# Performance work log

Hardware: AMD Instinct MI355X
Metric: run time of the kernel (lower is better)

## Reference

```python
import jax, jax.numpy as jnp
import numpy as np

B, N, C, K = 16, 2000, 4, 8
EPS = 1e-5


def setup_inputs() -> dict:
    key = jax.random.key(0)
    ks = jax.random.split(key, 10)
    def p(k, shape, s=0.1):
        return jax.random.normal(k, shape, jnp.float32) * s
    return {
        "data": jax.random.normal(ks[0], (B, 1, N, C), jnp.float32),
        "x": jax.random.normal(ks[1], (B, 1, N, 4), jnp.float32),
        "w1a": p(ks[2], (128, C)), "b1a": jnp.zeros((128,), jnp.float32),
        "w1b": p(ks[3], (128, 128)), "b1b": jnp.zeros((128,), jnp.float32),
        "w2": p(ks[4], (128, 2 * C + 2)), "b2": jnp.zeros((128,), jnp.float32),
        "res_wa": p(ks[5], (4, 128, 128)), "res_ba": jnp.zeros((4, 128), jnp.float32),
        "res_wb": p(ks[6], (4, 128, 128)), "res_bb": jnp.zeros((4, 128), jnp.float32),
        "wl": p(ks[7], (1, 128)), "bl": jnp.zeros((1,), jnp.float32),
    }


def conv1x1(t, w, b):
    # t: [B, Cin, H, W], w: [Cout, Cin]
    return jnp.einsum('bchw,oc->bohw', t, w) + b[None, :, None, None]


def bn(t):
    # training-mode BatchNorm2d, gamma=1 beta=0 (default init)
    m = jnp.mean(t, axis=(0, 2, 3), keepdims=True)
    v = jnp.var(t, axis=(0, 2, 3), keepdims=True)
    return (t - m) * jax.lax.rsqrt(v + EPS)


def instn(t):
    # InstanceNorm2d, affine=False
    m = jnp.mean(t, axis=(2, 3), keepdims=True)
    v = jnp.var(t, axis=(2, 3), keepdims=True)
    return (t - m) * jax.lax.rsqrt(v + EPS)


def res_block(t, wa, ba, wb, bb):
    h = jax.nn.relu(bn(instn(conv1x1(t, wa, ba))))
    h = bn(instn(conv1x1(h, wb, bb)))
    return jax.nn.relu(h + t)


def knn_idx(f, k):
    # f: [B, D, N]; negative squared distance, top-(k+1), drop self
    xx = jnp.sum(f * f, axis=1)                        # [B, N]
    inner = jnp.einsum('bdn,bdm->bnm', f, f)           # [B, N, N]
    pd = 2.0 * inner - xx[:, :, None] - xx[:, None, :]
    idx = jax.lax.top_k(pd, k + 1)[1]                  # [B, N, k+1]
    return idx[:, :, 1:]


def graph_feature(f, idx):
    # f: [B, D, N], idx: [B, N, k] -> [B, 2D, N, k]
    xf = jnp.transpose(f, (0, 2, 1))                   # [B, N, D]
    nb = jax.vmap(lambda a, i: a[i])(xf, idx)          # [B, N, k, D]
    xt = xf[:, :, None, :]
    gf = jnp.concatenate([jnp.broadcast_to(xt, nb.shape), xt - nb], axis=-1)
    return jnp.transpose(gf, (0, 3, 1, 2))


def reference(data, x, w1a, b1a, w1b, b1b, w2, b2,
              res_wa, res_ba, res_wb, res_bb, wl, bl):
    n = data.shape[2]
    t = jnp.transpose(data, (0, 3, 2, 1))              # [B, C, N, 1]

    # self_attention
    h = conv1x1(t, w1a, b1a)
    h = jax.nn.relu(bn(h))
    h = conv1x1(h, w1b, b1b)[..., 0]                   # [B, 128, N]
    h = h / (jnp.linalg.norm(h, axis=1, keepdims=True) + 1e-5)
    A_rowsum = jnp.einsum('bcn,bcm->bm', h, h)         # sum_i A[i, j]
    D = (A_rowsum - 1.0) / n                           # [B, N] (eye subtraction)
    feat = jnp.concatenate(
        [t, jax.nn.relu(jnp.tanh(D))[:, None, :, None]], axis=1)  # [B, C+1, N, 1]

    f = feat[..., 0]                                   # [B, C+1, N]
    idx = knn_idx(f, K)
    g = graph_feature(f, idx)                          # [B, 2C+2, N, K]

    out = jax.nn.relu(bn(conv1x1(g, w2, b2)))          # [B, 128, N, K]
    out = jnp.max(out, axis=-1, keepdims=True)         # [B, 128, N, 1]

    for i in range(4):
        out = res_block(out, res_wa[i], res_ba[i], res_wb[i], res_bb[i])

    logit = conv1x1(out, wl, bl)[:, 0, :, 0]           # [B, N]

    # weighted 8-point
    weights = jax.nn.relu(jnp.tanh(logit))             # [B, N]
    xp = jnp.transpose(x[:, 0], (0, 2, 1))             # [B, 4, N]
    ones = jnp.ones_like(xp[:, 0])
    X = jnp.stack([xp[:, 2] * xp[:, 0], xp[:, 2] * xp[:, 1], xp[:, 2],
                   xp[:, 3] * xp[:, 0], xp[:, 3] * xp[:, 1], xp[:, 3],
                   xp[:, 0], xp[:, 1], ones], axis=1)  # [B, 9, N]
    X = jnp.transpose(X, (0, 2, 1))                    # [B, N, 9]
    XwX = jnp.einsum('bnp,bnq->bpq', X, weights[:, :, None] * X)  # [B, 9, 9]
    _, v = jnp.linalg.eigh(XwX)                        # ascending eigvals
    e_hat = v[:, :, 0]                                 # smallest-eig eigenvector
    e_hat = e_hat / jnp.linalg.norm(e_hat, axis=1, keepdims=True)

    return (D, logit, e_hat)
```

## Files before the change

### kernel.cpp

```cpp
#include <hip/hip_runtime.h>
#include <math.h>

#define BB 16
#define NN 2000
#define CH 128
#define KNN 8
#define JCH 8
#define JSZ 250

__device__ inline float wred(float v) {
    for (int off = 32; off > 0; off >>= 1) v += __shfl_down(v, off, 64);
    return v;
}

__global__ void k_build_t(const float* __restrict__ data, float* __restrict__ t) {
    int i = blockIdx.x * 256 + threadIdx.x;
    if (i >= BB * 4 * NN) return;
    int n = i % NN;
    int c = (i / NN) & 3;
    int b = i / (4 * NN);
    t[i] = data[(b * NN + n) * 4 + c];
}

__global__ void k_conv1(const float* __restrict__ t, const float* __restrict__ w1a,
                        const float* __restrict__ b1a, float* __restrict__ c1) {
    int i = blockIdx.x * 256 + threadIdx.x;
    if (i >= BB * CH * NN) return;
    int n = i % NN;
    int rest = i / NN;
    int o = rest & 127;
    int b = rest >> 7;
    float acc = b1a[o];
    for (int c = 0; c < 4; ++c) acc += w1a[o * 4 + c] * t[(b * 4 + c) * NN + n];
    c1[i] = acc;
}

__global__ void k_chanstats(const float* __restrict__ src, float* __restrict__ chAB) {
    int o = blockIdx.x;
    int tid = threadIdx.x;
    float s = 0.f, ss = 0.f;
    for (int b = 0; b < BB; ++b) {
        const float* p = src + (b * CH + o) * NN;
        for (int n = tid; n < NN; n += 256) { float v = p[n]; s += v; ss += v * v; }
    }
    s = wred(s); ss = wred(ss);
    __shared__ float sh[8];
    int wid = tid >> 6, lane = tid & 63;
    if (lane == 0) { sh[wid] = s; sh[4 + wid] = ss; }
    __syncthreads();
    if (tid == 0) {
        float S0 = sh[0] + sh[1] + sh[2] + sh[3];
        float SS = sh[4] + sh[5] + sh[6] + sh[7];
        float m = S0 / (float)(BB * NN);
        float var = SS / (float)(BB * NN) - m * m;
        float a = rsqrtf(var + 1e-5f);
        chAB[o] = a;
        chAB[CH + o] = -m * a;
    }
}

__global__ __launch_bounds__(256) void k_gemm(const float* __restrict__ X, const float* __restrict__ W,
                                              const float* __restrict__ bias, float* __restrict__ Y,
                                              const float* __restrict__ ab, int mode) {
    int ot = blockIdx.x, by = blockIdx.y;
    int b = by >> 5, nt = by & 31;
    int n0 = nt * 64, o0 = ot * 64;
    int tid = threadIdx.x;
    int tx = tid & 15, ty = tid >> 4;
    __shared__ float Xs[32][64];
    __shared__ float Ws[32][68];
    float acc[4][4] = {};
    for (int jc = 0; jc < 4; ++jc) {
        for (int q = 0; q < 8; ++q) {
            int e = q * 256 + tid;
            int jj = e >> 6, nn = e & 63;
            int j = jc * 32 + jj, n = n0 + nn;
            float v = 0.f;
            if (n < NN) {
                v = X[(b * CH + j) * NN + n];
                if (mode == 1) v = fmaxf(ab[j] * v + ab[CH + j], 0.f);
                else if (mode == 2) { int bc = b * CH + j; v = fmaxf(ab[bc * 2] * v + ab[bc * 2 + 1], 0.f); }
            }
            Xs[jj][nn] = v;
        }
        for (int q = 0; q < 8; ++q) {
            int e = q * 256 + tid;
            int jj = e & 31, oo = e >> 5;
            Ws[jj][oo] = W[(o0 + oo) * CH + jc * 32 + jj];
        }
        __syncthreads();
        for (int jj = 0; jj < 32; ++jj) {
            float4 wv = *(const float4*)&Ws[jj][ty * 4];
            float4 xv = *(const float4*)&Xs[jj][tx * 4];
            float wva[4] = {wv.x, wv.y, wv.z, wv.w};
            float xva[4] = {xv.x, xv.y, xv.z, xv.w};
#pragma unroll
            for (int a = 0; a < 4; ++a)
#pragma unroll
                for (int bq = 0; bq < 4; ++bq) acc[a][bq] += wva[a] * xva[bq];
        }
        __syncthreads();
    }
    for (int a = 0; a < 4; ++a) {
        int o = o0 + ty * 4 + a;
        float bi = bias[o];
        for (int q = 0; q < 4; ++q) {
            int n = n0 + tx * 4 + q;
            if (n < NN) Y[(b * CH + o) * NN + n] = acc[a][q] + bi;
        }
    }
}

__global__ void k_invn(const float* __restrict__ h2, float* __restrict__ invn) {
    int b = blockIdx.x >> 3, chunk = blockIdx.x & 7;
    int n = chunk * 256 + threadIdx.x;
    if (n >= NN) return;
    float acc = 0.f;
    for (int c = 0; c < CH; ++c) { float v = h2[(b * CH + c) * NN + n]; acc += v * v; }
    invn[b * NN + n] = 1.f / (sqrtf(acc) + 1e-5f);
}

__global__ void k_S(const float* __restrict__ h2, const float* __restrict__ invn, float* __restrict__ Sv) {
    int row = blockIdx.x;
    int b = row >> 7;
    const float* p = h2 + row * NN;
    const float* iv = invn + b * NN;
    float s = 0.f;
    for (int n = threadIdx.x; n < NN; n += 256) s += p[n] * iv[n];
    s = wred(s);
    __shared__ float sh[4];
    int wid = threadIdx.x >> 6, lane = threadIdx.x & 63;
    if (lane == 0) sh[wid] = s;
    __syncthreads();
    if (threadIdx.x == 0) Sv[row] = sh[0] + sh[1] + sh[2] + sh[3];
}

__global__ void k_Df(const float* __restrict__ h2, const float* __restrict__ invn,
                     const float* __restrict__ Sv, const float* __restrict__ t,
                     float* __restrict__ outD, float* __restrict__ f5) {
    int b = blockIdx.x >> 3, chunk = blockIdx.x & 7;
    int n = chunk * 256 + threadIdx.x;
    if (n >= NN) return;
    float acc = 0.f;
    for (int c = 0; c < CH; ++c) acc += h2[(b * CH + c) * NN + n] * Sv[b * CH + c];
    float Ar = acc * invn[b * NN + n];
    float Dv = (Ar - 1.0f) / (float)NN;
    outD[b * NN + n] = Dv;
    for (int c = 0; c < 4; ++c) f5[(b * 5 + c) * NN + n] = t[(b * 4 + c) * NN + n];
    f5[(b * 5 + 4) * NN + n] = fmaxf(tanhf(Dv), 0.f);
}

__global__ __launch_bounds__(256) void k_knn_part(const float* __restrict__ f5,
                                                  float* __restrict__ pd, int* __restrict__ pj) {
    __shared__ float4 fs4[JSZ];
    __shared__ float fs1[JSZ];
    int jc = blockIdx.x, ic = blockIdx.y, b = blockIdx.z;
    int j0 = jc * JSZ;
    int tid = threadIdx.x;
    const float* fb = f5 + b * 5 * NN;
    for (int e = tid; e < JSZ; e += 256) {
        float4 v;
        v.x = fb[0 * NN + j0 + e];
        v.y = fb[1 * NN + j0 + e];
        v.z = fb[2 * NN + j0 + e];
        v.w = fb[3 * NN + j0 + e];
        fs4[e] = v;
        fs1[e] = fb[4 * NN + j0 + e];
    }
    __syncthreads();
    int i = ic * 256 + tid;
    if (i >= NN) return;
    float fi0 = fb[i], fi1 = fb[NN + i], fi2 = fb[2 * NN + i], fi3 = fb[3 * NN + i], fi4 = fb[4 * NN + i];
    float bd[8]; int bj[8];
#pragma unroll
    for (int q = 0; q < 8; ++q) { bd[q] = 1e30f; bj[q] = 0x7fffffff; }
    for (int jj = 0; jj < JSZ; ++jj) {
        float4 fj = fs4[jj];
        float fj4 = fs1[jj];
        int j = j0 + jj;
        float d0 = fi0 - fj.x, d1 = fi1 - fj.y, d2 = fi2 - fj.z;
        float d3 = fi3 - fj.w, d4 = fi4 - fj4;
        float d = d0 * d0 + d1 * d1 + d2 * d2 + d3 * d3 + d4 * d4;
        if (j != i && d < bd[7]) {
            float cd = d; int cj = j;
#pragma unroll
            for (int q = 0; q < 8; ++q) {
                bool lt = cd < bd[q];
                float td = lt ? bd[q] : cd;
                int tj = lt ? bj[q] : cj;
                bd[q] = lt ? cd : bd[q];
                bj[q] = lt ? cj : bj[q];
                cd = td; cj = tj;
            }
        }
    }
    long base = ((long)(b * NN + i) * JCH + jc) * 8;
#pragma unroll
    for (int q = 0; q < 8; ++q) { pd[base + q] = bd[q]; pj[base + q] = bj[q]; }
}

__global__ __launch_bounds__(256) void k_knn_merge(const float* __restrict__ pd, const int* __restrict__ pj,
                                                   int* __restrict__ idxb) {
    int s = blockIdx.x * 256 + threadIdx.x;
    if (s >= BB * NN) return;
    const float* dl = pd + (long)s * JCH * 8;
    const int* jl = pj + (long)s * JCH * 8;
    int ptr[JCH];
#pragma unroll
    for (int c = 0; c < JCH; ++c) ptr[c] = 0;
    for (int q = 0; q < 8; ++q) {
        float best = 1e38f; int bestj = 0x7fffffff; int bc = 0;
#pragma unroll
        for (int c = 0; c < JCH; ++c) {
            if (ptr[c] < 8) {
                float d = dl[c * 8 + ptr[c]];
                int j = jl[c * 8 + ptr[c]];
                if (d < best || (d == best && j < bestj)) { best = d; bestj = j; bc = c; }
            }
        }
        idxb[s * 8 + q] = bestj;
        ++ptr[bc];
    }
}

__global__ __launch_bounds__(256) void k_gstats(const float* __restrict__ f5, const int* __restrict__ idxb,
                                                double* __restrict__ gacc) {
    int s = blockIdx.x * 256 + threadIdx.x;
    float acc[65];
#pragma unroll
    for (int q = 0; q < 65; ++q) acc[q] = 0.f;
    if (s < BB * NN) {
        int b = s / NN, n = s - b * NN;
        float fo[5];
#pragma unroll
        for (int c = 0; c < 5; ++c) fo[c] = f5[(b * 5 + c) * NN + n];
        float sd[5] = {0, 0, 0, 0, 0};
        float sdd[15];
#pragma unroll
        for (int q = 0; q < 15; ++q) sdd[q] = 0.f;
        for (int k = 0; k < 8; ++k) {
            int j = idxb[s * 8 + k];
            float df[5];
#pragma unroll
            for (int c = 0; c < 5; ++c) df[c] = fo[c] - f5[(b * 5 + c) * NN + j];
#pragma unroll
            for (int c = 0; c < 5; ++c) sd[c] += df[c];
            int t = 0;
#pragma unroll
            for (int c = 0; c < 5; ++c)
#pragma unroll
                for (int d2 = c; d2 < 5; ++d2) { sdd[t] += df[c] * df[d2]; ++t; }
        }
#pragma unroll
        for (int c = 0; c < 5; ++c) { acc[c] = 8.f * fo[c]; acc[5 + c] = sd[c]; }
        int t = 10, sc = 0;
        for (int p = 0; p < 10; ++p)
            for (int q = p; q < 10; ++q) {
                float v;
                if (q < 5) v = 8.f * fo[p] * fo[q];
                else if (p < 5) v = fo[p] * sd[q - 5];
                else { v = sdd[sc]; ++sc; }
                acc[t++] = v;
            }
    }
#pragma unroll 1
    for (int q = 0; q < 65; ++q) {
        float v = acc[q];
        for (int off = 32; off > 0; off >>= 1) v += __shfl_down(v, off, 64);
        acc[q] = v;
    }
    __shared__ float sh[4][65];
    int lane = threadIdx.x & 63, wid = threadIdx.x >> 6;
    if (lane == 0) {
        for (int q = 0; q < 65; ++q) sh[wid][q] = acc[q];
    }
    __syncthreads();
    if (threadIdx.x < 65) {
        float tot = sh[0][threadIdx.x] + sh[1][threadIdx.x] + sh[2][threadIdx.x] + sh[3][threadIdx.x];
        atomicAdd(&gacc[threadIdx.x], (double)tot);
    }
}

__global__ void k_gfinal(const double* __restrict__ gacc, const float* __restrict__ w2,
                         const float* __restrict__ b2, float* __restrict__ g2ab) {
    int o = threadIdx.x;
    if (o >= 128) return;
    double inv = 1.0 / (double)(BB * NN * 8);
    double Wr[10];
    for (int c = 0; c < 10; ++c) Wr[c] = (double)w2[o * 10 + c];
    double gm[10];
    for (int c = 0; c < 10; ++c) gm[c] = gacc[c] * inv;
    double b0 = (double)b2[o];
    double mean = b0;
    for (int c = 0; c < 10; ++c) mean += Wr[c] * gm[c];
    double e2 = b0 * b0 + 2.0 * b0 * (mean - b0);
    int t = 10;
    for (int p = 0; p < 10; ++p)
        for (int q = p; q < 10; ++q) {
            double G = gacc[t] * inv; ++t;
            double contrib = Wr[p] * Wr[q] * G;
            e2 += (p == q) ? contrib : 2.0 * contrib;
        }
    double var = e2 - mean * mean;
    double a = 1.0 / sqrt(var + 1e-5);
    g2ab[o] = (float)a;
    g2ab[128 + o] = (float)(-mean * a);
}

__global__ __launch_bounds__(256) void k_graphconv(const float* __restrict__ f5, const int* __restrict__ idxb,
                                                   const float* __restrict__ w2, const float* __restrict__ b2,
                                                   const float* __restrict__ g2ab, float* __restrict__ x0) {
    __shared__ float ws[1280], bs[128];
    __shared__ float fo_s[16][5], fnb_s[16][8][5];
    __shared__ int idxs[16][8];
    int b = blockIdx.x / 125, tile = blockIdx.x % 125;
    int nbase = tile * 16;
    int tid = threadIdx.x;
    for (int e = tid; e < 1280; e += 256) ws[e] = w2[e];
    if (tid < 128) bs[tid] = b2[tid];
    if (tid < 128) { int nn = tid >> 3, k = tid & 7; idxs[nn][k] = idxb[(b * NN + nbase + nn) * 8 + k]; }
    if (tid >= 128 && tid < 208) { int e = tid - 128; int nn = e / 5, c = e % 5; fo_s[nn][c] = f5[(b * 5 + c) * NN + nbase + nn]; }
    __syncthreads();
    for (int e = tid; e < 640; e += 256) {
        int nn = e / 40, r = e % 40, k = r / 5, c = r % 5;
        fnb_s[nn][k][c] = f5[(b * 5 + c) * NN + idxs[nn][k]];
    }
    __syncthreads();
    int nn = tid & 15, og = tid >> 4;
    float fo[5];
#pragma unroll
    for (int c = 0; c < 5; ++c) fo[c] = fo_s[nn][c];
    for (int oo = 0; oo < 8; ++oo) {
        int o = og * 8 + oo;
        float base = bs[o];
        float wn[5];
#pragma unroll
        for (int c = 0; c < 5; ++c) {
            float w1 = ws[o * 10 + c], w5 = ws[o * 10 + 5 + c];
            base += (w1 + w5) * fo[c];
            wn[c] = w5;
        }
        float mx = -1e30f;
        for (int k = 0; k < 8; ++k) {
            float v = base;
#pragma unroll
            for (int c = 0; c < 5; ++c) v -= wn[c] * fnb_s[nn][k][c];
            mx = fmaxf(mx, v);
        }
        float y = fmaxf(g2ab[o] * mx + g2ab[128 + o], 0.f);
        x0[(b * CH + o) * NN + nbase + nn] = y;
    }
}

__global__ void k_rowstats(const float* __restrict__ src, float* __restrict__ stats) {
    int row = blockIdx.x;
    const float* p = src + row * NN;
    float s = 0.f, ss = 0.f;
    for (int n = threadIdx.x; n < NN; n += 256) { float v = p[n]; s += v; ss += v * v; }
    s = wred(s); ss = wred(ss);
    __shared__ float sh[8];
    int wid = threadIdx.x >> 6, lane = threadIdx.x & 63;
    if (lane == 0) { sh[wid] = s; sh[4 + wid] = ss; }
    __syncthreads();
    if (threadIdx.x == 0) {
        float S0 = sh[0] + sh[1] + sh[2] + sh[3];
        float SS = sh[4] + sh[5] + sh[6] + sh[7];
        float m = S0 / (float)NN;
        float var = SS / (float)NN - m * m;
        stats[row * 2] = m;
        stats[row * 2 + 1] = var;
    }
}

__global__ void k_finalize(const float* __restrict__ stats, float* __restrict__ ab) {
    int c = threadIdx.x;
    if (c >= 128) return;
    float acc = 0.f;
    for (int b = 0; b < BB; ++b) { float var = stats[(b * CH + c) * 2 + 1]; acc += var / (var + 1e-5f); }
    float vc = acc / (float)BB;
    float sc = rsqrtf(vc + 1e-5f);
    for (int b = 0; b < BB; ++b) {
        float m = stats[(b * CH + c) * 2];
        float var = stats[(b * CH + c) * 2 + 1];
        float a = rsqrtf(var + 1e-5f) * sc;
        ab[(b * CH + c) * 2] = a;
        ab[(b * CH + c) * 2 + 1] = -m * a;
    }
}

__global__ void k_resadd(const float* __restrict__ Bm, const float* __restrict__ ab,
                         const float* __restrict__ x, float* __restrict__ y) {
    int i = blockIdx.x * 256 + threadIdx.x;
    if (i >= BB * CH * NN) return;
    int bc = i / NN;
    float v = ab[bc * 2] * Bm[i] + ab[bc * 2 + 1] + x[i];
    y[i] = fmaxf(v, 0.f);
}

__global__ void k_logit(const float* __restrict__ x4, const float* __restrict__ wl,
                        const float* __restrict__ bl, float* __restrict__ outLogit) {
    int b = blockIdx.x >> 3, chunk = blockIdx.x & 7;
    int n = chunk * 256 + threadIdx.x;
    if (n >= NN) return;
    float acc = 0.f;
    for (int c = 0; c < CH; ++c) acc += wl[c] * x4[(b * CH + c) * NN + n];
    outLogit[b * NN + n] = acc + bl[0];
}

__global__ __launch_bounds__(256) void k_xwx(const float* __restrict__ logit, const float* __restrict__ x_in,
                                             float* __restrict__ XwX) {
    int b = blockIdx.x;
    int tid = threadIdx.x;
    float a[45];
#pragma unroll
    for (int q = 0; q < 45; ++q) a[q] = 0.f;
    for (int n = tid; n < NN; n += 256) {
        float lg = logit[b * NN + n];
        float w = fmaxf(tanhf(lg), 0.f);
        const float* xp = x_in + (b * NN + n) * 4;
        float px = xp[0], py = xp[1], z = xp[2], wq = xp[3];
        float X9[9] = {z * px, z * py, z, wq * px, wq * py, wq, px, py, 1.f};
        int t = 0;
#pragma unroll
        for (int p = 0; p < 9; ++p) {
            float wp = w * X9[p];
#pragma unroll
            for (int q = p; q < 9; ++q) { a[t] += wp * X9[q]; ++t; }
        }
    }
#pragma unroll 1
    for (int q = 0; q < 45; ++q) {
        float v = a[q];
        for (int off = 32; off > 0; off >>= 1) v += __shfl_down(v, off, 64);
        a[q] = v;
    }
    __shared__ float sh[4][45];
    int lane = tid & 63, wid = tid >> 6;
    if (lane == 0) {
        for (int q = 0; q < 45; ++q) sh[wid][q] = a[q];
    }
    __syncthreads();
    if (tid < 45) XwX[b * 45 + tid] = sh[0][tid] + sh[1][tid] + sh[2][tid] + sh[3][tid];
}

__device__ inline float slapy2_f(float x, float y) {
    float xa = fabsf(x), ya = fabsf(y);
    float w = fmaxf(xa, ya), z = fminf(xa, ya);
    if (z == 0.f) return w;
    float q = z / w;
    return w * sqrtf(1.f + q * q);
}

__device__ inline void slartg_f(float f, float g, float& c, float& s, float& r) {
    if (g == 0.f) { c = 1.f; s = 0.f; r = f; }
    else if (f == 0.f) { c = 0.f; s = (g > 0.f ? 1.f : -1.f); r = fabsf(g); }
    else {
        float d = sqrtf(f * f + g * g);
        c = fabsf(f) / d;
        r = (f >= 0.f) ? d : -d;
        s = g / r;
    }
}

__device__ void slaev2_f(float a, float b, float c, float& rt1, float& rt2, float& cs1, float& sn1) {
    float sm = a + c, df = a - c;
    float adf = fabsf(df), tb = b + b, ab = fabsf(tb);
    float acmx, acmn;
    if (fabsf(a) > fabsf(c)) { acmx = a; acmn = c; } else { acmx = c; acmn = a; }
    float rt;
    if (adf > ab) { float q = ab / adf; rt = adf * sqrtf(1.f + q * q); }
    else if (adf < ab) { float q = adf / ab; rt = ab * sqrtf(1.f + q * q); }
    else rt = ab * sqrtf(2.f);
    int sgn1;
    if (sm < 0.f) { rt1 = 0.5f * (sm - rt); sgn1 = -1; rt2 = (acmx / rt1) * acmn - (b / rt1) * b; }
    else if (sm > 0.f) { rt1 = 0.5f * (sm + rt); sgn1 = 1; rt2 = (acmx / rt1) * acmn - (b / rt1) * b; }
    else { rt1 = 0.5f * rt; rt2 = -0.5f * rt; sgn1 = 1; }
    float cs; int sgn2;
    if (df >= 0.f) { cs = df + rt; sgn2 = 1; } else { cs = df - rt; sgn2 = -1; }
    float acs = fabsf(cs);
    if (acs > ab) {
        float ct = -tb / cs;
        sn1 = 1.f / sqrtf(1.f + ct * ct);
        cs1 = ct * sn1;
    } else {
        if (ab == 0.f) { cs1 = 1.f; sn1 = 0.f; }
        else { float tn = -cs / tb; cs1 = 1.f / sqrtf(1.f + tn * tn); sn1 = tn * cs1; }
    }
    if (sgn1 == sgn2) { float tn = cs1; cs1 = -sn1; sn1 = tn; }
}

#define ROTLOG_MAX 2560

__global__ __launch_bounds__(64) void k_eigh(const float* __restrict__ XwX, float* __restrict__ out_e) {
    __shared__ float Am[81];
    __shared__ float dsh[9], esh[9], tsh[9];
    __shared__ float rc[ROTLOG_MAX], rs[ROTLOG_MAX];
    __shared__ int rj[ROTLOG_MAX];
    int bb = blockIdx.x;
    if (threadIdx.x != 0) return;
    float* d = dsh;
    float* e = esh;
    float* tau = tsh;
    int cnt = 0;
#define AA(i, j) Am[(i) * 9 + (j)]
    {
        const float* src = XwX + bb * 45;
        int t = 0;
        for (int p = 0; p < 9; ++p)
            for (int q = p; q < 9; ++q) { float v = src[t++]; AA(p, q) = v; AA(q, p) = v; }
    }
    for (int i = 0; i < 8; ++i) {
        float alpha = AA(i + 1, i);
        float xn2 = 0.f;
        for (int j = i + 2; j < 9; ++j) xn2 += AA(j, i) * AA(j, i);
        float taui;
        if (xn2 == 0.f) { taui = 0.f; e[i] = alpha; }
        else {
            float xnorm = sqrtf(xn2);
            float beta = slapy2_f(alpha, xnorm);
            beta = (alpha >= 0.f) ? -beta : beta;
            taui = (beta - alpha) / beta;
            float scl = 1.f / (alpha - beta);
            for (int j = i + 2; j < 9; ++j) AA(j, i) *= scl;
            e[i] = beta;
            float p[9], w[9];
            for (int j = i + 1; j < 9; ++j) {
                float acc = AA(j, i + 1);
                for (int k2 = i + 2; k2 < 9; ++k2) acc += AA(j, k2) * AA(k2, i);
                p[j] = taui * acc;
            }
            float dot = p[i + 1];
            for (int j = i + 2; j < 9; ++j) dot += p[j] * AA(j, i);
            float alpha2 = -0.5f * taui * dot;
            w[i + 1] = p[i + 1] + alpha2;
            for (int j = i + 2; j < 9; ++j) w[j] = p[j] + alpha2 * AA(j, i);
            for (int j = i + 1; j < 9; ++j) {
                float vj = (j == i + 1) ? 1.f : AA(j, i);
                for (int k2 = i + 1; k2 < 9; ++k2) {
                    float vk = (k2 == i + 1) ? 1.f : AA(k2, i);
                    AA(j, k2) -= vj * w[k2] + w[j] * vk;
                }
            }
        }
        tau[i] = taui;
    }
    for (int i = 0; i < 9; ++i) d[i] = AA(i, i);
    const float eps = 5.9604645e-08f;
    const float eps2 = 3.5527137e-15f;
    const float safmin = 1.17549435e-38f;
    const int n = 9;
    int nmaxit = n * 30, jtot = 0;
    int l1 = 0;
    while (l1 <= n - 1) {
        if (l1 > 0) e[l1 - 1] = 0.f;
        int m = n - 1;
        for (int mm = l1; mm <= n - 2; ++mm) {
            float tst = fabsf(e[mm]);
            if (tst == 0.f) { m = mm; break; }
            if (tst <= (sqrtf(fabsf(d[mm])) * sqrtf(fabsf(d[mm + 1]))) * eps) { e[mm] = 0.f; m = mm; break; }
        }
        int l = l1, lsv = l, lend = m, lendsv = lend;
        l1 = m + 1;
        if (lend == l) continue;
        if (fabsf(d[lend]) < fabsf(d[l])) { lend = lsv; l = lendsv; }
        if (lend > l) {
            for (;;) {
                int m2 = lend;
                if (l != lend) {
                    for (int mm = l; mm <= lend - 1; ++mm) {
                        float tst = e[mm] * e[mm];
                        if (tst <= (eps2 * fabsf(d[mm])) * fabsf(d[mm + 1]) + safmin) { m2 = mm; break; }
                    }
                }
                if (m2 < lend) e[m2] = 0.f;
                float p = d[l];
                if (m2 == l) { d[l] = p; ++l; if (l <= lend) continue; else break; }
                if (m2 == l + 1) {
                    float rt1, rt2, c, s;
                    slaev2_f(d[l], e[l], d[l + 1], rt1, rt2, c, s);
                    rc[cnt] = c; rs[cnt] = s; rj[cnt] = l; ++cnt;
                    d[l] = rt1; d[l + 1] = rt2; e[l] = 0.f; l += 2;
                    if (l <= lend) continue; else break;
                }
                if (jtot == nmaxit) break;
                ++jtot;
                float g = (d[l + 1] - p) / (2.f * e[l]);
                float r = slapy2_f(g, 1.f);
                g = d[m2] - p + e[l] / (g + (g >= 0.f ? fabsf(r) : -fabsf(r)));
                float s = 1.f, c = 1.f;
                p = 0.f;
                for (int i = m2 - 1; i >= l; --i) {
                    float f = s * e[i], bq = c * e[i];
                    slartg_f(g, f, c, s, r);
                    if (i != m2 - 1) e[i + 1] = r;
                    g = d[i + 1] - p;
                    r = (d[i] - g) * s + 2.f * c * bq;
                    p = s * r;
                    d[i + 1] = g + p;
                    g = c * r - bq;
                    rc[cnt] = c; rs[cnt] = -s; rj[cnt] = i; ++cnt;
                }
                d[l] -= p; e[l] = g;
            }
        } else {
            for (;;) {
                int m2 = lend;
                if (l != lend) {
                    for (int mm = l; mm >= lend + 1; --mm) {
                        float tst = e[mm - 1] * e[mm - 1];
                        if (tst <= (eps2 * fabsf(d[mm])) * fabsf(d[mm - 1]) + safmin) { m2 = mm; break; }
                    }
                }
                if (m2 > lend) e[m2 - 1] = 0.f;
                float p = d[l];
                if (m2 == l) { d[l] = p; --l; if (l >= lend) continue; else break; }
                if (m2 == l - 1) {
                    float rt1, rt2, c, s;
                    slaev2_f(d[l - 1], e[l - 1], d[l], rt1, rt2, c, s);
                    rc[cnt] = c; rs[cnt] = s; rj[cnt] = l - 1; ++cnt;
                    d[l - 1] = rt1; d[l] = rt2; e[l - 1] = 0.f; l -= 2;
                    if (l >= lend) continue; else break;
                }
                if (jtot == nmaxit) break;
                ++jtot;
                float g = (d[l - 1] - p) / (2.f * e[l - 1]);
                float r = slapy2_f(g, 1.f);
                g = d[m2] - p + e[l - 1] / (g + (g >= 0.f ? fabsf(r) : -fabsf(r)));
                float s = 1.f, c = 1.f;
                p = 0.f;
                for (int i = m2; i <= l - 1; ++i) {
                    float f = s * e[i], bq = c * e[i];
                    slartg_f(g, f, c, s, r);
                    if (i != m2) e[i - 1] = r;
                    g = d[i] - p;
                    r = (d[i + 1] - g) * s + 2.f * c * bq;
                    p = s * r;
                    d[i] = g + p;
                    g = c * r - bq;
                    rc[cnt] = c; rs[cnt] = s; rj[cnt] = i; ++cnt;
                }
                d[l] -= p; e[l - 1] = g;
            }
        }
    }
    int perm[9];
    for (int i = 0; i < 9; ++i) perm[i] = i;
    for (int ii = 1; ii < 9; ++ii) {
        int i = ii - 1, kk = i;
        float p = d[i];
        for (int j = ii; j < 9; ++j)
            if (d[j] < p) { kk = j; p = d[j]; }
        if (kk != i) {
            d[kk] = d[i]; d[i] = p;
            int tp = perm[i]; perm[i] = perm[kk]; perm[kk] = tp;
        }
    }
    int kcol = perm[0];
    float w0 = (kcol == 0) ? 1.f : 0.f, w1 = (kcol == 1) ? 1.f : 0.f, w2 = (kcol == 2) ? 1.f : 0.f;
    float w3 = (kcol == 3) ? 1.f : 0.f, w4 = (kcol == 4) ? 1.f : 0.f, w5 = (kcol == 5) ? 1.f : 0.f;
    float w6 = (kcol == 6) ? 1.f : 0.f, w7 = (kcol == 7) ? 1.f : 0.f, w8 = (kcol == 8) ? 1.f : 0.f;
    for (int t = cnt - 1; t >= 0; --t) {
        float c = rc[t], s = rs[t];
        int j = rj[t];
        switch (j) {
            case 0: { float a = w0, b = w1; w0 = c * a - s * b; w1 = s * a + c * b; } break;
            case 1: { float a = w1, b = w2; w1 = c * a - s * b; w2 = s * a + c * b; } break;
            case 2: { float a = w2, b = w3; w2 = c * a - s * b; w3 = s * a + c * b; } break;
            case 3: { float a = w3, b = w4; w3 = c * a - s * b; w4 = s * a + c * b; } break;
            case 4: { float a = w4, b = w5; w4 = c * a - s * b; w5 = s * a + c * b; } break;
            case 5: { float a = w5, b = w6; w5 = c * a - s * b; w6 = s * a + c * b; } break;
            case 6: { float a = w6, b = w7; w6 = c * a - s * b; w7 = s * a + c * b; } break;
            default: { float a = w7, b = w8; w7 = c * a - s * b; w8 = s * a + c * b; } break;
        }
    }
    float v0[9] = {w0, w1, w2, w3, w4, w5, w6, w7, w8};
    for (int i = 7; i >= 0; --i) {
        float ti = tau[i];
        if (ti == 0.f) continue;
        float dot = v0[i + 1];
        for (int j = i + 2; j < 9; ++j) dot += AA(j, i) * v0[j];
        dot *= ti;
        v0[i + 1] -= dot;
        for (int j = i + 2; j < 9; ++j) v0[j] -= AA(j, i) * dot;
    }
    float nrm = 0.f;
    for (int r2 = 0; r2 < 9; ++r2) nrm += v0[r2] * v0[r2];
    nrm = sqrtf(nrm);
    for (int r2 = 0; r2 < 9; ++r2) out_e[bb * 9 + r2] = v0[r2] / nrm;
#undef AA
}

extern "C" void kernel_launch(void* const* d_in, const int* in_sizes, int n_in,
                              void* d_out, int out_size, void* d_ws, size_t ws_size,
                              hipStream_t stream) {
    const float* data = (const float*)d_in[0];
    const float* x_in = (const float*)d_in[1];
    const float* w1a = (const float*)d_in[2];
    const float* b1a = (const float*)d_in[3];
    const float* w1b = (const float*)d_in[4];
    const float* b1b = (const float*)d_in[5];
    const float* w2 = (const float*)d_in[6];
    const float* b2 = (const float*)d_in[7];
    const float* res_wa = (const float*)d_in[8];
    const float* res_ba = (const float*)d_in[9];
    const float* res_wb = (const float*)d_in[10];
    const float* res_bb = (const float*)d_in[11];
    const float* wl = (const float*)d_in[12];
    const float* bl = (const float*)d_in[13];
    float* out = (float*)d_out;

    double* gacc = (double*)d_ws;
    float* xwx = (float*)((char*)d_ws + 1024);
    float* fbase = (float*)((char*)d_ws + 8192);
    float* big0 = fbase;
    float* big1 = big0 + BB * CH * NN;
    float* big2 = big1 + BB * CH * NN;
    float* tbuf = big2 + BB * CH * NN;
    float* f5 = tbuf + BB * 4 * NN;
    float* invn = f5 + BB * 5 * NN;
    float* Sv = invn + BB * NN;
    int* idxb = (int*)(Sv + BB * CH);
    float* chAB = (float*)(idxb + BB * NN * 8);
    float* stA = chAB + 256;
    float* abA = stA + BB * CH * 2;
    float* stB = abA + BB * CH * 2;
    float* abB = stB + BB * CH * 2;
    float* g2ab = abB + BB * CH * 2;
    float* knn_pd = big2;
    int* knn_pj = (int*)(big2 + BB * NN * JCH * 8);

    hipMemsetAsync(d_ws, 0, 1024, stream);

    k_build_t<<<500, 256, 0, stream>>>(data, tbuf);
    k_conv1<<<16000, 256, 0, stream>>>(tbuf, w1a, b1a, big0);
    k_chanstats<<<128, 256, 0, stream>>>(big0, chAB);
    k_gemm<<<dim3(2, 512), 256, 0, stream>>>(big0, w1b, b1b, big1, chAB, 1);
    k_invn<<<128, 256, 0, stream>>>(big1, invn);
    k_S<<<2048, 256, 0, stream>>>(big1, invn, Sv);
    k_Df<<<128, 256, 0, stream>>>(big1, invn, Sv, tbuf, out, f5);
    k_knn_part<<<dim3(JCH, 8, BB), 256, 0, stream>>>(f5, knn_pd, knn_pj);
    k_knn_merge<<<125, 256, 0, stream>>>(knn_pd, knn_pj, idxb);
    k_gstats<<<125, 256, 0, stream>>>(f5, idxb, gacc);
    k_gfinal<<<1, 128, 0, stream>>>(gacc, w2, b2, g2ab);
    k_graphconv<<<2000, 256, 0, stream>>>(f5, idxb, w2, b2, g2ab, big0);

    float* xb = big0;
    float* hb = big1;
    for (int i = 0; i < 4; ++i) {
        k_gemm<<<dim3(2, 512), 256, 0, stream>>>(xb, res_wa + i * CH * CH, res_ba + i * CH, hb, nullptr, 0);
        k_rowstats<<<2048, 256, 0, stream>>>(hb, stA);
        k_finalize<<<1, 128, 0, stream>>>(stA, abA);
        k_gemm<<<dim3(2, 512), 256, 0, stream>>>(hb, res_wb + i * CH * CH, res_bb + i * CH, big2, abA, 2);
        k_rowstats<<<2048, 256, 0, stream>>>(big2, stB);
        k_finalize<<<1, 128, 0, stream>>>(stB, abB);
        k_resadd<<<16000, 256, 0, stream>>>(big2, abB, xb, hb);
        float* tmp = xb; xb = hb; hb = tmp;
    }

    k_logit<<<128, 256, 0, stream>>>(xb, wl, bl, out + BB * NN);
    k_xwx<<<16, 256, 0, stream>>>(out + BB * NN, x_in, xwx);
    k_eigh<<<16, 64, 0, stream>>>(xwx, out + 2 * BB * NN);
}
```

Baseline: 843.7 us.

## Fuse row stats, BN finalize and residual add; drop the input transpose kernel

Removes the separate transpose kernel: conv1 and the D/f5 kernel now read the channel-last input directly. In each residual block, the per-row stats, batch finalize and residual add/ReLU kernels are merged into one per-channel kernel, launched with 128 blocks, that computes stats, finalizes the scales and optionally applies the residual add. This cuts launches and intermediate stat buffers. The price is far less parallelism: 128 blocks instead of 2048 or 16000, each walking 16 rows in sequence with block syncs, which can leave much of the GPU idle.

Result: slower. 1.206 ms (+43.0%).

```diff
diff --git a/kernel.cpp b/kernel.cpp
--- a/kernel.cpp
+++ b/kernel.cpp
@@ -13,16 +13,7 @@
     return v;
 }
 
-__global__ void k_build_t(const float* __restrict__ data, float* __restrict__ t) {
-    int i = blockIdx.x * 256 + threadIdx.x;
-    if (i >= BB * 4 * NN) return;
-    int n = i % NN;
-    int c = (i / NN) & 3;
-    int b = i / (4 * NN);
-    t[i] = data[(b * NN + n) * 4 + c];
-}
-
-__global__ void k_conv1(const float* __restrict__ t, const float* __restrict__ w1a,
+__global__ void k_conv1(const float* __restrict__ data, const float* __restrict__ w1a,
                         const float* __restrict__ b1a, float* __restrict__ c1) {
     int i = blockIdx.x * 256 + threadIdx.x;
     if (i >= BB * CH * NN) return;
@@ -30,8 +21,9 @@
     int rest = i / NN;
     int o = rest & 127;
     int b = rest >> 7;
+    const float* dp = data + (b * NN + n) * 4;
     float acc = b1a[o];
-    for (int c = 0; c < 4; ++c) acc += w1a[o * 4 + c] * t[(b * 4 + c) * NN + n];
+    for (int c = 0; c < 4; ++c) acc += w1a[o * 4 + c] * dp[c];
     c1[i] = acc;
 }
 
@@ -136,7 +128,7 @@
 }
 
 __global__ void k_Df(const float* __restrict__ h2, const float* __restrict__ invn,
-                     const float* __restrict__ Sv, const float* __restrict__ t,
+                     const float* __restrict__ Sv, const float* __restrict__ data,
                      float* __restrict__ outD, float* __restrict__ f5) {
     int b = blockIdx.x >> 3, chunk = blockIdx.x & 7;
     int n = chunk * 256 + threadIdx.x;
@@ -146,7 +138,8 @@
     float Ar = acc * invn[b * NN + n];
     float Dv = (Ar - 1.0f) / (float)NN;
     outD[b * NN + n] = Dv;
-    for (int c = 0; c < 4; ++c) f5[(b * 5 + c) * NN + n] = t[(b * 4 + c) * NN + n];
+    const float* dp = data + (b * NN + n) * 4;
+    for (int c = 0; c < 4; ++c) f5[(b * 5 + c) * NN + n] = dp[c];
     f5[(b * 5 + 4) * NN + n] = fmaxf(tanhf(Dv), 0.f);
 }
 
@@ -352,49 +345,58 @@
     }
 }
 
-__global__ void k_rowstats(const float* __restrict__ src, float* __restrict__ stats) {
-    int row = blockIdx.x;
-    const float* p = src + row * NN;
-    float s = 0.f, ss = 0.f;
-    for (int n = threadIdx.x; n < NN; n += 256) { float v = p[n]; s += v; ss += v * v; }
-    s = wred(s); ss = wred(ss);
+__global__ __launch_bounds__(256) void k_rowfin(const float* __restrict__ src, float* __restrict__ ab,
+                                                const float* __restrict__ x, float* __restrict__ xnext) {
+    int c = blockIdx.x;
+    int tid = threadIdx.x;
     __shared__ float sh[8];
-    int wid = threadIdx.x >> 6, lane = threadIdx.x & 63;
-    if (lane == 0) { sh[wid] = s; sh[4 + wid] = ss; }
+    __shared__ float mv[16][2];
+    __shared__ float abs_[16][2];
+    int wid = tid >> 6, lane = tid & 63;
+    for (int b = 0; b < BB; ++b) {
+        const float* p = src + (b * CH + c) * NN;
+        float s = 0.f, ss = 0.f;
+        for (int n = tid; n < NN; n += 256) { float v = p[n]; s += v; ss += v * v; }
+        s = wred(s); ss = wred(ss);
+        if (lane == 0) { sh[wid] = s; sh[4 + wid] = ss; }
+        __syncthreads();
+        if (tid == 0) {
+            float S0 = sh[0] + sh[1] + sh[2] + sh[3];
+            float SS = sh[4] + sh[5] + sh[6] + sh[7];
+            float m = S0 / (float)NN;
+            float var = SS / (float)NN - m * m;
+            mv[b][0] = m; mv[b][1] = var;
+        }
+        __syncthreads();
+    }
+    if (tid == 0) {
+        float acc = 0.f;
+        for (int b = 0; b < BB; ++b) { float var = mv[b][1]; acc += var / (var + 1e-5f); }
+        float vc = acc / (float)BB;
+        float sc = rsqrtf(vc + 1e-5f);
+        for (int b = 0; b < BB; ++b) {
+            float m = mv[b][0];
+            float var = mv[b][1];
+            float a = rsqrtf(var + 1e-5f) * sc;
+            abs_[b][0] = a;
+            abs_[b][1] = -m * a;
+            ab[(b * CH + c) * 2] = a;
+            ab[(b * CH + c) * 2 + 1] = -m * a;
+        }
+    }
     __syncthreads();
-    if (threadIdx.x == 0) {
-        float S0 = sh[0] + sh[1] + sh[2] + sh[3];
-        float SS = sh[4] + sh[5] + sh[6] + sh[7];
-        float m = S0 / (float)NN;
-        float var = SS / (float)NN - m * m;
-        stats[row * 2] = m;
-        stats[row * 2 + 1] = var;
-    }
-}
-
-__global__ void k_finalize(const float* __restrict__ stats, float* __restrict__ ab) {
-    int c = threadIdx.x;
-    if (c >= 128) return;
-    float acc = 0.f;
-    for (int b = 0; b < BB; ++b) { float var = stats[(b * CH + c) * 2 + 1]; acc += var / (var + 1e-5f); }
-    float vc = acc / (float)BB;
-    float sc = rsqrtf(vc + 1e-5f);
-    for (int b = 0; b < BB; ++b) {
-        float m = stats[(b * CH + c) * 2];
-        float var = stats[(b * CH + c) * 2 + 1];
-        float a = rsqrtf(var + 1e-5f) * sc;
-        ab[(b * CH + c) * 2] = a;
-        ab[(b * CH + c) * 2 + 1] = -m * a;
-    }
-}
-
-__global__ void k_resadd(const float* __restrict__ Bm, const float* __restrict__ ab,
-                         const float* __restrict__ x, float* __restrict__ y) {
-    int i = blockIdx.x * 256 + threadIdx.x;
-    if (i >= BB * CH * NN) return;
-    int bc = i / NN;
-    float v = ab[bc * 2] * Bm[i] + ab[bc * 2 + 1] + x[i];
-    y[i] = fmaxf(v, 0.f);
+    if (xnext != nullptr) {
+        for (int b = 0; b < BB; ++b) {
+            float a = abs_[b][0], bi = abs_[b][1];
+            const float* pB = src + (b * CH + c) * NN;
+            const float* pX = x + (b * CH + c) * NN;
+            float* pY = xnext + (b * CH + c) * NN;
+            for (int n = tid; n < NN; n += 256) {
+                float v = a * pB[n] + bi + pX[n];
+                pY[n] = fmaxf(v, 0.f);
+            }
+        }
+    }
 }
 
 __global__ void k_logit(const float* __restrict__ x4, const float* __restrict__ wl,
@@ -731,13 +733,12 @@
 
     hipMemsetAsync(d_ws, 0, 1024, stream);
 
-    k_build_t<<<500, 256, 0, stream>>>(data, tbuf);
-    k_conv1<<<16000, 256, 0, stream>>>(tbuf, w1a, b1a, big0);
+    k_conv1<<<16000, 256, 0, stream>>>(data, w1a, b1a, big0);
     k_chanstats<<<128, 256, 0, stream>>>(big0, chAB);
     k_gemm<<<dim3(2, 512), 256, 0, stream>>>(big0, w1b, b1b, big1, chAB, 1);
     k_invn<<<128, 256, 0, stream>>>(big1, invn);
     k_S<<<2048, 256, 0, stream>>>(big1, invn, Sv);
-    k_Df<<<128, 256, 0, stream>>>(big1, invn, Sv, tbuf, out, f5);
+    k_Df<<<128, 256, 0, stream>>>(big1, invn, Sv, data, out, f5);
     k_knn_part<<<dim3(JCH, 8, BB), 256, 0, stream>>>(f5, knn_pd, knn_pj);
     k_knn_merge<<<125, 256, 0, stream>>>(knn_pd, knn_pj, idxb);
     k_gstats<<<125, 256, 0, stream>>>(f5, idxb, gacc);
@@ -748,12 +749,9 @@
     float* hb = big1;
     for (int i = 0; i < 4; ++i) {
         k_gemm<<<dim3(2, 512), 256, 0, stream>>>(xb, res_wa + i * CH * CH, res_ba + i * CH, hb, nullptr, 0);
-        k_rowstats<<<2048, 256, 0, stream>>>(hb, stA);
-        k_finalize<<<1, 128, 0, stream>>>(stA, abA);
+        k_rowfin<<<128, 256, 0, stream>>>(hb, abA, nullptr, nullptr);
         k_gemm<<<dim3(2, 512), 256, 0, stream>>>(hb, res_wb + i * CH * CH, res_bb + i * CH, big2, abA, 2);
-        k_rowstats<<<2048, 256, 0, stream>>>(big2, stB);
-        k_finalize<<<1, 128, 0, stream>>>(stB, abB);
-        k_resadd<<<16000, 256, 0, stream>>>(big2, abB, xb, hb);
+        k_rowfin<<<128, 256, 0, stream>>>(big2, abB, xb, hb);
         float* tmp = xb; xb = hb; hb = tmp;
     }
 
```

## Drop transpose kernel, fuse logit into XwX, run eigh state in wave registers

Applied to the files above, without the earlier changes.

Removes the k_build_t transpose by having conv1 and Df read the interleaved input directly. Folds the logit projection into the XwX reduction kernel, saving one launch and a round trip of the logit through memory. Moves the eigensolver's d/e/tau arrays and eigenvector into per-lane registers accessed through readlane, with wave reductions for the back-transform. In exchange, the logit work now runs on only 16 blocks instead of 128, and the Householder update adds two barriers per matrix element.

New measurement: 1.065 ms. +26.2%, slower.

```diff
diff --git a/kernel.cpp b/kernel.cpp
--- a/kernel.cpp
+++ b/kernel.cpp
@@ -13,16 +13,7 @@
     return v;
 }
 
-__global__ void k_build_t(const float* __restrict__ data, float* __restrict__ t) {
-    int i = blockIdx.x * 256 + threadIdx.x;
-    if (i >= BB * 4 * NN) return;
-    int n = i % NN;
-    int c = (i / NN) & 3;
-    int b = i / (4 * NN);
-    t[i] = data[(b * NN + n) * 4 + c];
-}
-
-__global__ void k_conv1(const float* __restrict__ t, const float* __restrict__ w1a,
+__global__ void k_conv1(const float* __restrict__ data, const float* __restrict__ w1a,
                         const float* __restrict__ b1a, float* __restrict__ c1) {
     int i = blockIdx.x * 256 + threadIdx.x;
     if (i >= BB * CH * NN) return;
@@ -30,8 +21,9 @@
     int rest = i / NN;
     int o = rest & 127;
     int b = rest >> 7;
+    const float* dp = data + (b * NN + n) * 4;
     float acc = b1a[o];
-    for (int c = 0; c < 4; ++c) acc += w1a[o * 4 + c] * t[(b * 4 + c) * NN + n];
+    for (int c = 0; c < 4; ++c) acc += w1a[o * 4 + c] * dp[c];
     c1[i] = acc;
 }
 
@@ -136,7 +128,7 @@
 }
 
 __global__ void k_Df(const float* __restrict__ h2, const float* __restrict__ invn,
-                     const float* __restrict__ Sv, const float* __restrict__ t,
+                     const float* __restrict__ Sv, const float* __restrict__ data,
                      float* __restrict__ outD, float* __restrict__ f5) {
     int b = blockIdx.x >> 3, chunk = blockIdx.x & 7;
     int n = chunk * 256 + threadIdx.x;
@@ -146,7 +138,8 @@
     float Ar = acc * invn[b * NN + n];
     float Dv = (Ar - 1.0f) / (float)NN;
     outD[b * NN + n] = Dv;
-    for (int c = 0; c < 4; ++c) f5[(b * 5 + c) * NN + n] = t[(b * 4 + c) * NN + n];
+    const float* dp = data + (b * NN + n) * 4;
+    for (int c = 0; c < 4; ++c) f5[(b * 5 + c) * NN + n] = dp[c];
     f5[(b * 5 + 4) * NN + n] = fmaxf(tanhf(Dv), 0.f);
 }
 
@@ -397,25 +390,19 @@
     y[i] = fmaxf(v, 0.f);
 }
 
-__global__ void k_logit(const float* __restrict__ x4, const float* __restrict__ wl,
-                        const float* __restrict__ bl, float* __restrict__ outLogit) {
-    int b = blockIdx.x >> 3, chunk = blockIdx.x & 7;
-    int n = chunk * 256 + threadIdx.x;
-    if (n >= NN) return;
-    float acc = 0.f;
-    for (int c = 0; c < CH; ++c) acc += wl[c] * x4[(b * CH + c) * NN + n];
-    outLogit[b * NN + n] = acc + bl[0];
-}
-
-__global__ __launch_bounds__(256) void k_xwx(const float* __restrict__ logit, const float* __restrict__ x_in,
-                                             float* __restrict__ XwX) {
+__global__ __launch_bounds__(256) void k_xwx(const float* __restrict__ x4, const float* __restrict__ wl,
+                                             const float* __restrict__ bl, const float* __restrict__ x_in,
+                                             float* __restrict__ outLogit, float* __restrict__ XwX) {
     int b = blockIdx.x;
     int tid = threadIdx.x;
     float a[45];
 #pragma unroll
     for (int q = 0; q < 45; ++q) a[q] = 0.f;
     for (int n = tid; n < NN; n += 256) {
-        float lg = logit[b * NN + n];
+        float acc = 0.f;
+        for (int c = 0; c < CH; ++c) acc += wl[c] * x4[(b * CH + c) * NN + n];
+        float lg = acc + bl[0];
+        outLogit[b * NN + n] = lg;
         float w = fmaxf(tanhf(lg), 0.f);
         const float* xp = x_in + (b * NN + n) * 4;
         float px = xp[0], py = xp[1], z = xp[2], wq = xp[3];
@@ -441,6 +428,14 @@
     }
     __syncthreads();
     if (tid < 45) XwX[b * 45 + tid] = sh[0][tid] + sh[1][tid] + sh[2][tid] + sh[3][tid];
+}
+
+__device__ __forceinline__ float lgetf(float reg, int i) {
+    return __int_as_float(__builtin_amdgcn_readlane(__float_as_int(reg), i));
+}
+__device__ __forceinline__ float wsum64(float v) {
+    for (int off = 32; off > 0; off >>= 1) v += __shfl_xor(v, off, 64);
+    return v;
 }
 
 __device__ inline float slapy2_f(float x, float y) {
@@ -493,28 +488,33 @@
 
 __global__ __launch_bounds__(64) void k_eigh(const float* __restrict__ XwX, float* __restrict__ out_e) {
     __shared__ float Am[81];
-    __shared__ float dsh[9], esh[9], tsh[9];
-    __shared__ float rc[ROTLOG_MAX], rs[ROTLOG_MAX];
-    __shared__ int rj[ROTLOG_MAX];
+    __shared__ float rcl[ROTLOG_MAX], rsl[ROTLOG_MAX];
+    __shared__ int rjl[ROTLOG_MAX];
     int bb = blockIdx.x;
-    if (threadIdx.x != 0) return;
-    float* d = dsh;
-    float* e = esh;
-    float* tau = tsh;
-    int cnt = 0;
+    int lane = threadIdx.x;
 #define AA(i, j) Am[(i) * 9 + (j)]
+#define DGET(i) lgetf(dreg, (i))
+#define DSET(i, v) do { float _v = (v); dreg = (lane == (i)) ? _v : dreg; } while (0)
+#define EGET(i) lgetf(ereg, (i))
+#define ESET(i, v) do { float _v = (v); ereg = (lane == (i)) ? _v : ereg; } while (0)
     {
         const float* src = XwX + bb * 45;
-        int t = 0;
-        for (int p = 0; p < 9; ++p)
-            for (int q = p; q < 9; ++q) { float v = src[t++]; AA(p, q) = v; AA(q, p) = v; }
-    }
+        for (int e2 = lane; e2 < 81; e2 += 64) {
+            int r0 = e2 / 9, c0 = e2 % 9;
+            int a0 = r0 < c0 ? r0 : c0, b0 = r0 < c0 ? c0 : r0;
+            int t = a0 * 9 - (a0 * (a0 - 1)) / 2 + (b0 - a0);
+            Am[e2] = src[t];
+        }
+    }
+    __syncthreads();
+    float dreg = 0.f, ereg = 0.f, treg = 0.f;
+    int cnt = 0;
     for (int i = 0; i < 8; ++i) {
         float alpha = AA(i + 1, i);
         float xn2 = 0.f;
         for (int j = i + 2; j < 9; ++j) xn2 += AA(j, i) * AA(j, i);
         float taui;
-        if (xn2 == 0.f) { taui = 0.f; e[i] = alpha; }
+        if (xn2 == 0.f) { taui = 0.f; ESET(i, alpha); }
         else {
             float xnorm = sqrtf(xn2);
             float beta = slapy2_f(alpha, xnorm);
@@ -522,7 +522,7 @@
             taui = (beta - alpha) / beta;
             float scl = 1.f / (alpha - beta);
             for (int j = i + 2; j < 9; ++j) AA(j, i) *= scl;
-            e[i] = beta;
+            ESET(i, beta);
             float p[9], w[9];
             for (int j = i + 1; j < 9; ++j) {
                 float acc = AA(j, i + 1);
@@ -538,13 +538,16 @@
                 float vj = (j == i + 1) ? 1.f : AA(j, i);
                 for (int k2 = i + 1; k2 < 9; ++k2) {
                     float vk = (k2 == i + 1) ? 1.f : AA(k2, i);
-                    AA(j, k2) -= vj * w[k2] + w[j] * vk;
+                    float upd = AA(j, k2) - (vj * w[k2] + w[j] * vk);
+                    __syncthreads();
+                    if (lane == 0) AA(j, k2) = upd;
+                    __syncthreads();
                 }
             }
         }
-        tau[i] = taui;
-    }
-    for (int i = 0; i < 9; ++i) d[i] = AA(i, i);
+        treg = (lane == i) ? taui : treg;
+    }
+    dreg = (lane < 9) ? Am[lane * 10] : 0.f;
     const float eps = 5.9604645e-08f;
     const float eps2 = 3.5527137e-15f;
     const float safmin = 1.17549435e-38f;
@@ -552,142 +555,157 @@
     int nmaxit = n * 30, jtot = 0;
     int l1 = 0;
     while (l1 <= n - 1) {
-        if (l1 > 0) e[l1 - 1] = 0.f;
+        if (l1 > 0) ESET(l1 - 1, 0.f);
         int m = n - 1;
         for (int mm = l1; mm <= n - 2; ++mm) {
-            float tst = fabsf(e[mm]);
+            float tst = fabsf(EGET(mm));
             if (tst == 0.f) { m = mm; break; }
-            if (tst <= (sqrtf(fabsf(d[mm])) * sqrtf(fabsf(d[mm + 1]))) * eps) { e[mm] = 0.f; m = mm; break; }
+            if (tst <= (sqrtf(fabsf(DGET(mm))) * sqrtf(fabsf(DGET(mm + 1)))) * eps) { ESET(mm, 0.f); m = mm; break; }
         }
         int l = l1, lsv = l, lend = m, lendsv = lend;
         l1 = m + 1;
         if (lend == l) continue;
-        if (fabsf(d[lend]) < fabsf(d[l])) { lend = lsv; l = lendsv; }
+        if (fabsf(DGET(lend)) < fabsf(DGET(l))) { lend = lsv; l = lendsv; }
         if (lend > l) {
             for (;;) {
                 int m2 = lend;
                 if (l != lend) {
                     for (int mm = l; mm <= lend - 1; ++mm) {
-                        float tst = e[mm] * e[mm];
-                        if (tst <= (eps2 * fabsf(d[mm])) * fabsf(d[mm + 1]) + safmin) { m2 = mm; break; }
+                        float em = EGET(mm);
+                        float tst = em * em;
+                        if (tst <= (eps2 * fabsf(DGET(mm))) * fabsf(DGET(mm + 1)) + safmin) { m2 = mm; break; }
                     }
                 }
-                if (m2 < lend) e[m2] = 0.f;
-                float p = d[l];
-                if (m2 == l) { d[l] = p; ++l; if (l <= lend) continue; else break; }
+                if (m2 < lend) ESET(m2, 0.f);
+                float p = DGET(l);
+                if (m2 == l) { DSET(l, p); ++l; if (l <= lend) continue; else break; }
                 if (m2 == l + 1) {
                     float rt1, rt2, c, s;
-                    slaev2_f(d[l], e[l], d[l + 1], rt1, rt2, c, s);
-                    rc[cnt] = c; rs[cnt] = s; rj[cnt] = l; ++cnt;
-                    d[l] = rt1; d[l + 1] = rt2; e[l] = 0.f; l += 2;
+                    slaev2_f(DGET(l), EGET(l), DGET(l + 1), rt1, rt2, c, s);
+                    if (lane == 0) { rcl[cnt] = c; rsl[cnt] = s; rjl[cnt] = l; }
+                    ++cnt;
+                    DSET(l, rt1); DSET(l + 1, rt2); ESET(l, 0.f); l += 2;
                     if (l <= lend) continue; else break;
                 }
                 if (jtot == nmaxit) break;
                 ++jtot;
-                float g = (d[l + 1] - p) / (2.f * e[l]);
+                float g = (DGET(l + 1) - p) / (2.f * EGET(l));
                 float r = slapy2_f(g, 1.f);
-                g = d[m2] - p + e[l] / (g + (g >= 0.f ? fabsf(r) : -fabsf(r)));
+                g = DGET(m2) - p + EGET(l) / (g + (g >= 0.f ? fabsf(r) : -fabsf(r)));
                 float s = 1.f, c = 1.f;
                 p = 0.f;
                 for (int i = m2 - 1; i >= l; --i) {
-                    float f = s * e[i], bq = c * e[i];
+                    float ei = EGET(i);
+                    float f = s * ei, bq = c * ei;
                     slartg_f(g, f, c, s, r);
-                    if (i != m2 - 1) e[i + 1] = r;
-                    g = d[i + 1] - p;
-                    r = (d[i] - g) * s + 2.f * c * bq;
+                    if (i != m2 - 1) ESET(i + 1, r);
+                    g = DGET(i + 1) - p;
+                    r = (DGET(i) - g) * s + 2.f * c * bq;
                     p = s * r;
-                    d[i + 1] = g + p;
+                    DSET(i + 1, g + p);
                     g = c * r - bq;
-                    rc[cnt] = c; rs[cnt] = -s; rj[cnt] = i; ++cnt;
+                    if (lane == 0) { rcl[cnt] = c; rsl[cnt] = -s; rjl[cnt] = i; }
+                    ++cnt;
                 }
-                d[l] -= p; e[l] = g;
+                DSET(l, DGET(l) - p);
+                ESET(l, g);
             }
         } else {
             for (;;) {
                 int m2 = lend;
                 if (l != lend) {
                     for (int mm = l; mm >= lend + 1; --mm) {
-                        float tst = e[mm - 1] * e[mm - 1];
-                        if (tst <= (eps2 * fabsf(d[mm])) * fabsf(d[mm - 1]) + safmin) { m2 = mm; break; }
+                        float em = EGET(mm - 1);
+                        float tst = em * em;
+                        if (tst <= (eps2 * fabsf(DGET(mm))) * fabsf(DGET(mm - 1)) + safmin) { m2 = mm; break; }
                     }
                 }
-                if (m2 > lend) e[m2 - 1] = 0.f;
-                float p = d[l];
-                if (m2 == l) { d[l] = p; --l; if (l >= lend) continue; else break; }
+                if (m2 > lend) ESET(m2 - 1, 0.f);
+                float p = DGET(l);
+                if (m2 == l) { DSET(l, p); --l; if (l >= lend) continue; else break; }
                 if (m2 == l - 1) {
                     float rt1, rt2, c, s;
-                    slaev2_f(d[l - 1], e[l - 1], d[l], rt1, rt2, c, s);
-                    rc[cnt] = c; rs[cnt] = s; rj[cnt] = l - 1; ++cnt;
-                    d[l - 1] = rt1; d[l] = rt2; e[l - 1] = 0.f; l -= 2;
+                    slaev2_f(DGET(l - 1), EGET(l - 1), DGET(l), rt1, rt2, c, s);
+                    if (lane == 0) { rcl[cnt] = c; rsl[cnt] = s; rjl[cnt] = l - 1; }
+                    ++cnt;
+                    DSET(l - 1, rt1); DSET(l, rt2); ESET(l - 1, 0.f); l -= 2;
                     if (l >= lend) continue; else break;
                 }
                 if (jtot == nmaxit) break;
                 ++jtot;
-                float g = (d[l - 1] - p) / (2.f * e[l - 1]);
+                float g = (DGET(l - 1) - p) / (2.f * EGET(l - 1));
                 float r = slapy2_f(g, 1.f);
-                g = d[m2] - p + e[l - 1] / (g + (g >= 0.f ? fabsf(r) : -fabsf(r)));
+                g = DGET(m2) - p + EGET(l - 1) / (g + (g >= 0.f ? fabsf(r) : -fabsf(r)));
                 float s = 1.f, c = 1.f;
                 p = 0.f;
                 for (int i = m2; i <= l - 1; ++i) {
-                    float f = s * e[i], bq = c * e[i];
+                    float ei = EGET(i);
+                    float f = s * ei, bq = c * ei;
                     slartg_f(g, f, c, s, r);
-                    if (i != m2) e[i - 1] = r;
-                    g = d[i] - p;
-                    r = (d[i + 1] - g) * s + 2.f * c * bq;
+                    if (i != m2) ESET(i - 1, r);
+                    g = DGET(i) - p;
+                    r = (DGET(i + 1) - g) * s + 2.f * c * bq;
                     p = s * r;
-                    d[i] = g + p;
+                    DSET(i, g + p);
                     g = c * r - bq;
-                    rc[cnt] = c; rs[cnt] = s; rj[cnt] = i; ++cnt;
+                    if (lane == 0) { rcl[cnt] = c; rsl[cnt] = s; rjl[cnt] = i; }
+                    ++cnt;
                 }
-                d[l] -= p; e[l - 1] = g;
+                DSET(l, DGET(l) - p);
+                ESET(l - 1, g);
             }
         }
     }
-    int perm[9];
-    for (int i = 0; i < 9; ++i) perm[i] = i;
+    __syncthreads();
+    int permreg = lane;
     for (int ii = 1; ii < 9; ++ii) {
         int i = ii - 1, kk = i;
-        float p = d[i];
-        for (int j = ii; j < 9; ++j)
-            if (d[j] < p) { kk = j; p = d[j]; }
+        float p = DGET(i);
+        for (int j = ii; j < 9; ++j) {
+            float dj = DGET(j);
+            if (dj < p) { kk = j; p = dj; }
+        }
         if (kk != i) {
-            d[kk] = d[i]; d[i] = p;
-            int tp = perm[i]; perm[i] = perm[kk]; perm[kk] = tp;
-        }
-    }
-    int kcol = perm[0];
-    float w0 = (kcol == 0) ? 1.f : 0.f, w1 = (kcol == 1) ? 1.f : 0.f, w2 = (kcol == 2) ? 1.f : 0.f;
-    float w3 = (kcol == 3) ? 1.f : 0.f, w4 = (kcol == 4) ? 1.f : 0.f, w5 = (kcol == 5) ? 1.f : 0.f;
-    float w6 = (kcol == 6) ? 1.f : 0.f, w7 = (kcol == 7) ? 1.f : 0.f, w8 = (kcol == 8) ? 1.f : 0.f;
+            float di = DGET(i);
+            DSET(kk, di);
+            DSET(i, p);
+            int pi = __builtin_amdgcn_readlane(permreg, i);
+            int pk = __builtin_amdgcn_readlane(permreg, kk);
+            permreg = (lane == i) ? pk : permreg;
+            permreg = (lane == kk) ? pi : permreg;
+        }
+    }
+    int kcol = __builtin_amdgcn_readlane(permreg, 0);
+    float v0reg = (lane == kcol) ? 1.f : 0.f;
     for (int t = cnt - 1; t >= 0; --t) {
-        float c = rc[t], s = rs[t];
-        int j = rj[t];
-        switch (j) {
-            case 0: { float a = w0, b = w1; w0 = c * a - s * b; w1 = s * a + c * b; } break;
-            case 1: { float a = w1, b = w2; w1 = c * a - s * b; w2 = s * a + c * b; } break;
-            case 2: { float a = w2, b = w3; w2 = c * a - s * b; w3 = s * a + c * b; } break;
-            case 3: { float a = w3, b = w4; w3 = c * a - s * b; w4 = s * a + c * b; } break;
-            case 4: { float a = w4, b = w5; w4 = c * a - s * b; w5 = s * a + c * b; } break;
-            case 5: { float a = w5, b = w6; w5 = c * a - s * b; w6 = s * a + c * b; } break;
-            case 6: { float a = w6, b = w7; w6 = c * a - s * b; w7 = s * a + c * b; } break;
-            default: { float a = w7, b = w8; w7 = c * a - s * b; w8 = s * a + c * b; } break;
-        }
-    }
-    float v0[9] = {w0, w1, w2, w3, w4, w5, w6, w7, w8};
+        float c = rcl[t], s = rsl[t];
+        int j = rjl[t];
+        float a = lgetf(v0reg, j);
+        float b2 = lgetf(v0reg, j + 1);
+        float nj = c * a - s * b2;
+        float nj1 = s * a + c * b2;
+        v0reg = (lane == j) ? nj : v0reg;
+        v0reg = (lane == j + 1) ? nj1 : v0reg;
+    }
     for (int i = 7; i >= 0; --i) {
-        float ti = tau[i];
+        float ti = lgetf(treg, i);
         if (ti == 0.f) continue;
-        float dot = v0[i + 1];
-        for (int j = i + 2; j < 9; ++j) dot += AA(j, i) * v0[j];
-        dot *= ti;
-        v0[i + 1] -= dot;
-        for (int j = i + 2; j < 9; ++j) v0[j] -= AA(j, i) * dot;
-    }
-    float nrm = 0.f;
-    for (int r2 = 0; r2 < 9; ++r2) nrm += v0[r2] * v0[r2];
-    nrm = sqrtf(nrm);
-    for (int r2 = 0; r2 < 9; ++r2) out_e[bb * 9 + r2] = v0[r2] / nrm;
+        float avi = (lane >= i + 2 && lane <= 8) ? Am[lane * 9 + i] : 0.f;
+        float contrib = 0.f;
+        if (lane == i + 1) contrib = v0reg;
+        else if (lane >= i + 2 && lane <= 8) contrib = avi * v0reg;
+        float dot = wsum64(contrib) * ti;
+        if (lane == i + 1) v0reg -= dot;
+        else if (lane >= i + 2 && lane <= 8) v0reg -= avi * dot;
+    }
+    float sq = (lane < 9) ? v0reg * v0reg : 0.f;
+    float nrm = sqrtf(wsum64(sq));
+    if (lane < 9) out_e[bb * 9 + lane] = v0reg / nrm;
 #undef AA
+#undef DGET
+#undef DSET
+#undef EGET
+#undef ESET
 }
 
 extern "C" void kernel_launch(void* const* d_in, const int* in_sizes, int n_in,
@@ -731,13 +749,12 @@
 
     hipMemsetAsync(d_ws, 0, 1024, stream);
 
-    k_build_t<<<500, 256, 0, stream>>>(data, tbuf);
-    k_conv1<<<16000, 256, 0, stream>>>(tbuf, w1a, b1a, big0);
+    k_conv1<<<16000, 256, 0, stream>>>(data, w1a, b1a, big0);
     k_chanstats<<<128, 256, 0, stream>>>(big0, chAB);
     k_gemm<<<dim3(2, 512), 256, 0, stream>>>(big0, w1b, b1b, big1, chAB, 1);
     k_invn<<<128, 256, 0, stream>>>(big1, invn);
     k_S<<<2048, 256, 0, stream>>>(big1, invn, Sv);
-    k_Df<<<128, 256, 0, stream>>>(big1, invn, Sv, tbuf, out, f5);
+    k_Df<<<128, 256, 0, stream>>>(big1, invn, Sv, data, out, f5);
     k_knn_part<<<dim3(JCH, 8, BB), 256, 0, stream>>>(f5, knn_pd, knn_pj);
     k_knn_merge<<<125, 256, 0, stream>>>(knn_pd, knn_pj, idxb);
     k_gstats<<<125, 256, 0, stream>>>(f5, idxb, gacc);
@@ -757,7 +774,6 @@
         float* tmp = xb; xb = hb; hb = tmp;
     }
 
-    k_logit<<<128, 256, 0, stream>>>(xb, wl, bl, out + BB * NN);
-    k_xwx<<<16, 256, 0, stream>>>(out + BB * NN, x_in, xwx);
+    k_xwx<<<16, 256, 0, stream>>>(xb, wl, bl, x_in, out + BB * NN, xwx);
     k_eigh<<<16, 64, 0, stream>>>(xwx, out + 2 * BB * NN);
 }
```
